# Kernel optimization log

Measured on AMD Instinct MI355X. Metric: run time of the kernel, lower is better.

## Reference

```python
import jax, jax.numpy as jnp
import numpy as np

N = 8192
F_IN = 512
F_OUT = 512
DENSITY = 0.01


def setup_inputs() -> dict:
    key = jax.random.key(0)
    k_x, k_adj, k_w, k_b = jax.random.split(key, 4)
    input_features = jax.random.normal(k_x, (N, F_IN), dtype=jnp.float32)
    adj = (jax.random.uniform(k_adj, (N, N)) < DENSITY).astype(jnp.float32)
    idx = jnp.arange(N)
    adj = adj.at[idx, idx].set(1.0)
    # nn.Linear(in, out) params; W stored as [in, out] so hidden = x @ W + b
    W = jax.random.normal(k_w, (F_IN, F_OUT), dtype=jnp.float32) / np.sqrt(F_IN)
    b = jax.random.normal(k_b, (F_OUT,), dtype=jnp.float32) * 0.01
    return {"input_features": input_features, "adj": adj, "W": W, "b": b}


def reference(input_features, adj, W, b):
    # adj.to_dense().bool().float(): binarize any nonzero entry
    A = (adj != 0).astype(input_features.dtype)  # [N, N]
    hidden = input_features @ W + b              # [N, F_out]
    deg = jnp.sum(A, axis=0)                     # column sums, [N]
    return (A @ hidden) / deg[:, None]           # [N, F_out]
```

## Files before the change

### kernel.cpp

```cpp
#include <hip/hip_runtime.h>
#include <stdint.h>

#define N_NODES 8192
#define FEAT 512
#define QCAP 512

__device__ __forceinline__ unsigned short f2bf(float f) {
  unsigned int u = __float_as_uint(f);
  u += 0x7fffu + ((u >> 16) & 1u);
  return (unsigned short)(u >> 16);
}
__device__ __forceinline__ float bflo(unsigned int u) { return __uint_as_float(u << 16); }
__device__ __forceinline__ float bfhi(unsigned int u) { return __uint_as_float(u & 0xffff0000u); }

typedef __attribute__((ext_vector_type(8))) short short8;
typedef __attribute__((ext_vector_type(4))) float floatx4;

__global__ __launch_bounds__(256) void prep_kernel(const float* __restrict__ W,
                                                   unsigned short* __restrict__ Wt,
                                                   unsigned int* __restrict__ deg) {
  int gid = blockIdx.x * 256 + threadIdx.x;
  int k = gid >> 9, n = gid & 511;
  Wt[n * 512 + k] = f2bf(W[gid]);
  if (gid < N_NODES) deg[gid] = 0u;
}

__global__ __launch_bounds__(512) void gemm_kernel(const float* __restrict__ x,
                                                   const unsigned short* __restrict__ Wt,
                                                   const float* __restrict__ bias,
                                                   unsigned short* __restrict__ hidden) {
  __shared__ __align__(16) unsigned short Ab[64][40];
  __shared__ __align__(16) unsigned short Bb[256][40];
  int t = threadIdx.x;
  int m0 = blockIdx.x * 64;
  int n0 = blockIdx.y * 256;
  int lane = t & 63, wave = t >> 6;
  int quad = lane >> 4, l15 = lane & 15;
  int wm = wave & 1, wn = wave >> 1;

  floatx4 acc[2][4];
#pragma unroll
  for (int i = 0; i < 2; ++i)
#pragma unroll
    for (int j = 0; j < 4; ++j) acc[i][j] = (floatx4)0.0f;

  int ar = t >> 3, ac = (t & 7) * 4;
  int br = t >> 1, bc = (t & 1) * 16;
  const float* xa = x + (size_t)(m0 + ar) * 512 + ac;
  const unsigned short* wb = Wt + (size_t)(n0 + br) * 512 + bc;

  float4 av = *(const float4*)xa;
  uint4 bv0 = *(const uint4*)wb;
  uint4 bv1 = *(const uint4*)(wb + 8);

  for (int kt = 0; kt < 16; ++kt) {
    uint2 aw;
    aw.x = (unsigned int)f2bf(av.x) | ((unsigned int)f2bf(av.y) << 16);
    aw.y = (unsigned int)f2bf(av.z) | ((unsigned int)f2bf(av.w) << 16);
    __syncthreads();
    *(uint2*)&Ab[ar][ac] = aw;
    *(uint4*)&Bb[br][bc] = bv0;
    *(uint4*)&Bb[br][bc + 8] = bv1;
    if (kt < 15) {
      int k0 = (kt + 1) * 32;
      av  = *(const float4*)(xa + k0);
      bv0 = *(const uint4*)(wb + k0);
      bv1 = *(const uint4*)(wb + k0 + 8);
    }
    __syncthreads();

    short8 af[2];
    short8 bfr[4];
#pragma unroll
    for (int im = 0; im < 2; ++im)
      af[im] = *(const short8*)&Ab[wm * 32 + im * 16 + l15][quad * 8];
#pragma unroll
    for (int jn = 0; jn < 4; ++jn)
      bfr[jn] = *(const short8*)&Bb[wn * 64 + jn * 16 + l15][quad * 8];
#pragma unroll
    for (int im = 0; im < 2; ++im)
#pragma unroll
      for (int jn = 0; jn < 4; ++jn)
        acc[im][jn] = __builtin_amdgcn_mfma_f32_16x16x32_bf16(af[im], bfr[jn], acc[im][jn], 0, 0, 0);
  }

#pragma unroll
  for (int jn = 0; jn < 4; ++jn) {
    int col = n0 + wn * 64 + jn * 16 + l15;
    float bb = bias[col];
#pragma unroll
    for (int im = 0; im < 2; ++im) {
#pragma unroll
      for (int rg = 0; rg < 4; ++rg) {
        int row = m0 + wm * 32 + im * 16 + quad * 4 + rg;
        hidden[(size_t)row * 512 + col] = f2bf(acc[im][jn][rg] + bb);
      }
    }
  }
}

__global__ __launch_bounds__(512) void gather_kernel(const float* __restrict__ adj,
                                                     const unsigned short* __restrict__ hidden,
                                                     float* __restrict__ out,
                                                     unsigned int* __restrict__ deg) {
  __shared__ unsigned int degl[N_NODES];
  __shared__ unsigned short q[8][QCAP];
  int tid = threadIdx.x;
#pragma unroll
  for (int i = 0; i < 16; ++i) degl[i * 512 + tid] = 0u;
  __syncthreads();

  int lane = tid & 63, wave = tid >> 6;
  unsigned short* wq = q[wave];
  unsigned long long lanemask = (1ull << lane) - 1ull;
  int r = blockIdx.x * 8 + wave;

  const float4* __restrict__ arow = (const float4*)(adj + ((size_t)r << 13));
  int qcnt = 0;

  float4 c0 = arow[lane];
  float4 c1 = arow[64 + lane];
  for (int ch = 0; ch < 32; ++ch) {
    float4 nx = make_float4(0.f, 0.f, 0.f, 0.f);
    if (ch < 30) nx = arow[(ch + 2) * 64 + lane];
    int cbase = ch * 256 + 4 * lane;
#pragma unroll
    for (int e = 0; e < 4; ++e) {
      float val = (e == 0) ? c0.x : (e == 1) ? c0.y : (e == 2) ? c0.z : c0.w;
      bool nz = (val != 0.0f);
      unsigned long long m = __ballot(nz);
      if (nz) {
        atomicAdd(&degl[cbase + e], 1u);
        wq[qcnt + __popcll(m & lanemask)] = (unsigned short)(cbase + e);
      }
      qcnt += __popcll(m);
    }
    c0 = c1; c1 = nx;
  }

  float acc[8] = {0.f, 0.f, 0.f, 0.f, 0.f, 0.f, 0.f, 0.f};
  int qhead = 0;
  for (; qhead + 8 <= qcnt; qhead += 8) {
    int jj[8];
#pragma unroll
    for (int d = 0; d < 8; ++d) jj[d] = wq[qhead + d];
    uint4 h[8];
#pragma unroll
    for (int d = 0; d < 8; ++d)
      h[d] = ((const uint4*)(hidden + ((size_t)jj[d] << 9)))[lane];
#pragma unroll
    for (int d = 0; d < 8; ++d) {
      acc[0] += bflo(h[d].x); acc[1] += bfhi(h[d].x);
      acc[2] += bflo(h[d].y); acc[3] += bfhi(h[d].y);
      acc[4] += bflo(h[d].z); acc[5] += bfhi(h[d].z);
      acc[6] += bflo(h[d].w); acc[7] += bfhi(h[d].w);
    }
  }
  for (; qhead < qcnt; ++qhead) {
    int j = wq[qhead];
    uint4 h = ((const uint4*)(hidden + ((size_t)j << 9)))[lane];
    acc[0] += bflo(h.x); acc[1] += bfhi(h.x);
    acc[2] += bflo(h.y); acc[3] += bfhi(h.y);
    acc[4] += bflo(h.z); acc[5] += bfhi(h.z);
    acc[6] += bflo(h.w); acc[7] += bfhi(h.w);
  }

  float4* orow = (float4*)(out + ((size_t)r << 9));
  orow[2 * lane]     = make_float4(acc[0], acc[1], acc[2], acc[3]);
  orow[2 * lane + 1] = make_float4(acc[4], acc[5], acc[6], acc[7]);

  __syncthreads();
#pragma unroll
  for (int i = 0; i < 16; ++i) {
    unsigned int c = degl[i * 512 + tid];
    if (c) atomicAdd(&deg[i * 512 + tid], c);
  }
}

__global__ __launch_bounds__(256) void norm_kernel(float* __restrict__ out,
                                                   const unsigned int* __restrict__ deg) {
  int lane = threadIdx.x & 63, wave = threadIdx.x >> 6;
  int r = blockIdx.x * 4 + wave;
  float s = 1.0f / (float)deg[r];
  float4* p = (float4*)(out + ((size_t)r << 9));
  float4 v0 = p[lane], v1 = p[64 + lane];
  v0.x *= s; v0.y *= s; v0.z *= s; v0.w *= s;
  v1.x *= s; v1.y *= s; v1.z *= s; v1.w *= s;
  p[lane] = v0;
  p[64 + lane] = v1;
}

extern "C" void kernel_launch(void* const* d_in, const int* in_sizes, int n_in,
                              void* d_out, int out_size, void* d_ws, size_t ws_size,
                              hipStream_t stream) {
  const float* x   = (const float*)d_in[0];
  const float* adj = (const float*)d_in[1];
  const float* W   = (const float*)d_in[2];
  const float* b   = (const float*)d_in[3];
  float* out = (float*)d_out;

  char* ws = (char*)d_ws;
  unsigned short* hidden = (unsigned short*)ws;
  unsigned short* Wt     = (unsigned short*)(ws + (size_t)N_NODES * FEAT * 2);
  unsigned int*   deg    = (unsigned int*)(ws + (size_t)N_NODES * FEAT * 2 + (size_t)FEAT * FEAT * 2);

  prep_kernel<<<1024, 256, 0, stream>>>(W, Wt, deg);
  gemm_kernel<<<dim3(128, 2), 512, 0, stream>>>(x, Wt, b, hidden);
  gather_kernel<<<1024, 512, 0, stream>>>(adj, hidden, out, deg);
  norm_kernel<<<2048, 256, 0, stream>>>(out, deg);
}
```

Measured before the change: 426.5 us.

## Overlap GEMM with adjacency scan in one launch; fold normalization into gather

Merges the dense GEMM and the adjacency scan into one kernel launch. The first 256 blocks compute hidden while the remaining blocks scan the 256MB adjacency, write per-row neighbor queues to global memory and accumulate degrees. A separate drain kernel then gathers hidden rows and applies the 1/deg scaling directly, which removes the norm kernel and its extra read and write of the output. The aim is to hide the GEMM behind the bandwidth-bound adjacency read. The cost is a round trip of the queues through global memory.

```diff
diff --git a/kernel.cpp b/kernel.cpp
--- a/kernel.cpp
+++ b/kernel.cpp
@@ -25,120 +25,146 @@
   if (gid < N_NODES) deg[gid] = 0u;
 }
 
-__global__ __launch_bounds__(512) void gemm_kernel(const float* __restrict__ x,
-                                                   const unsigned short* __restrict__ Wt,
-                                                   const float* __restrict__ bias,
-                                                   unsigned short* __restrict__ hidden) {
-  __shared__ __align__(16) unsigned short Ab[64][40];
-  __shared__ __align__(16) unsigned short Bb[256][40];
+__global__ __launch_bounds__(512) void fused_kernel(const float* __restrict__ x,
+                                                    const unsigned short* __restrict__ Wt,
+                                                    const float* __restrict__ bias,
+                                                    unsigned short* __restrict__ hidden,
+                                                    const float* __restrict__ adj,
+                                                    unsigned short* __restrict__ gq,
+                                                    unsigned int* __restrict__ qlen,
+                                                    unsigned int* __restrict__ deg) {
+  __shared__ __align__(16) char smem[32768];
+  int b = blockIdx.x;
   int t = threadIdx.x;
-  int m0 = blockIdx.x * 64;
-  int n0 = blockIdx.y * 256;
   int lane = t & 63, wave = t >> 6;
-  int quad = lane >> 4, l15 = lane & 15;
-  int wm = wave & 1, wn = wave >> 1;
-
-  floatx4 acc[2][4];
-#pragma unroll
-  for (int i = 0; i < 2; ++i)
-#pragma unroll
-    for (int j = 0; j < 4; ++j) acc[i][j] = (floatx4)0.0f;
-
-  int ar = t >> 3, ac = (t & 7) * 4;
-  int br = t >> 1, bc = (t & 1) * 16;
-  const float* xa = x + (size_t)(m0 + ar) * 512 + ac;
-  const unsigned short* wb = Wt + (size_t)(n0 + br) * 512 + bc;
-
-  float4 av = *(const float4*)xa;
-  uint4 bv0 = *(const uint4*)wb;
-  uint4 bv1 = *(const uint4*)(wb + 8);
-
-  for (int kt = 0; kt < 16; ++kt) {
-    uint2 aw;
-    aw.x = (unsigned int)f2bf(av.x) | ((unsigned int)f2bf(av.y) << 16);
-    aw.y = (unsigned int)f2bf(av.z) | ((unsigned int)f2bf(av.w) << 16);
+
+  if (b < 256) {
+    unsigned short (*Ab)[40] = (unsigned short (*)[40])smem;
+    unsigned short (*Bb)[40] = (unsigned short (*)[40])(smem + 64 * 40 * 2);
+    int m0 = (b >> 1) * 64;
+    int n0 = (b & 1) * 256;
+    int quad = lane >> 4, l15 = lane & 15;
+    int wm = wave & 1, wn = wave >> 1;
+
+    floatx4 acc[2][4];
+#pragma unroll
+    for (int i = 0; i < 2; ++i)
+#pragma unroll
+      for (int j = 0; j < 4; ++j) acc[i][j] = (floatx4)0.0f;
+
+    int ar = t >> 3, ac = (t & 7) * 4;
+    int br = t >> 1, bc = (t & 1) * 16;
+    const float* xa = x + (size_t)(m0 + ar) * 512 + ac;
+    const unsigned short* wb = Wt + (size_t)(n0 + br) * 512 + bc;
+
+    float4 av = *(const float4*)xa;
+    uint4 bv0 = *(const uint4*)wb;
+    uint4 bv1 = *(const uint4*)(wb + 8);
+
+    for (int kt = 0; kt < 16; ++kt) {
+      uint2 aw;
+      aw.x = (unsigned int)f2bf(av.x) | ((unsigned int)f2bf(av.y) << 16);
+      aw.y = (unsigned int)f2bf(av.z) | ((unsigned int)f2bf(av.w) << 16);
+      __syncthreads();
+      *(uint2*)&Ab[ar][ac] = aw;
+      *(uint4*)&Bb[br][bc] = bv0;
+      *(uint4*)&Bb[br][bc + 8] = bv1;
+      if (kt < 15) {
+        int k0 = (kt + 1) * 32;
+        av  = *(const float4*)(xa + k0);
+        bv0 = *(const uint4*)(wb + k0);
+        bv1 = *(const uint4*)(wb + k0 + 8);
+      }
+      __syncthreads();
+
+      short8 af[2];
+      short8 bfr[4];
+#pragma unroll
+      for (int im = 0; im < 2; ++im)
+        af[im] = *(const short8*)&Ab[wm * 32 + im * 16 + l15][quad * 8];
+#pragma unroll
+      for (int jn = 0; jn < 4; ++jn)
+        bfr[jn] = *(const short8*)&Bb[wn * 64 + jn * 16 + l15][quad * 8];
+#pragma unroll
+      for (int im = 0; im < 2; ++im)
+#pragma unroll
+        for (int jn = 0; jn < 4; ++jn)
+          acc[im][jn] = __builtin_amdgcn_mfma_f32_16x16x32_bf16(af[im], bfr[jn], acc[im][jn], 0, 0, 0);
+    }
+
+#pragma unroll
+    for (int jn = 0; jn < 4; ++jn) {
+      int col = n0 + wn * 64 + jn * 16 + l15;
+      float bb = bias[col];
+#pragma unroll
+      for (int im = 0; im < 2; ++im) {
+#pragma unroll
+        for (int rg = 0; rg < 4; ++rg) {
+          int row = m0 + wm * 32 + im * 16 + quad * 4 + rg;
+          hidden[(size_t)row * 512 + col] = f2bf(acc[im][jn][rg] + bb);
+        }
+      }
+    }
+  } else {
+    unsigned int* degl = (unsigned int*)smem;
+#pragma unroll
+    for (int i = 0; i < 16; ++i) degl[i * 512 + t] = 0u;
     __syncthreads();
-    *(uint2*)&Ab[ar][ac] = aw;
-    *(uint4*)&Bb[br][bc] = bv0;
-    *(uint4*)&Bb[br][bc + 8] = bv1;
-    if (kt < 15) {
-      int k0 = (kt + 1) * 32;
-      av  = *(const float4*)(xa + k0);
-      bv0 = *(const uint4*)(wb + k0);
-      bv1 = *(const uint4*)(wb + k0 + 8);
-    }
+
+    int r = (b - 256) * 8 + wave;
+    unsigned short* wq = gq + (size_t)r * QCAP;
+    unsigned long long lanemask = (1ull << lane) - 1ull;
+    const float4* __restrict__ arow = (const float4*)(adj + ((size_t)r << 13));
+    int qcnt = 0;
+
+    float4 c0 = arow[lane];
+    float4 c1 = arow[64 + lane];
+    for (int ch = 0; ch < 32; ++ch) {
+      float4 nx = make_float4(0.f, 0.f, 0.f, 0.f);
+      if (ch < 30) nx = arow[(ch + 2) * 64 + lane];
+      int cbase = ch * 256 + 4 * lane;
+#pragma unroll
+      for (int e = 0; e < 4; ++e) {
+        float val = (e == 0) ? c0.x : (e == 1) ? c0.y : (e == 2) ? c0.z : c0.w;
+        bool nz = (val != 0.0f);
+        unsigned long long m = __ballot(nz);
+        if (nz) {
+          atomicAdd(&degl[cbase + e], 1u);
+          wq[qcnt + __popcll(m & lanemask)] = (unsigned short)(cbase + e);
+        }
+        qcnt += __popcll(m);
+      }
+      c0 = c1; c1 = nx;
+    }
+    if (lane == 0) qlen[r] = (unsigned int)qcnt;
+
     __syncthreads();
-
-    short8 af[2];
-    short8 bfr[4];
-#pragma unroll
-    for (int im = 0; im < 2; ++im)
-      af[im] = *(const short8*)&Ab[wm * 32 + im * 16 + l15][quad * 8];
-#pragma unroll
-    for (int jn = 0; jn < 4; ++jn)
-      bfr[jn] = *(const short8*)&Bb[wn * 64 + jn * 16 + l15][quad * 8];
-#pragma unroll
-    for (int im = 0; im < 2; ++im)
-#pragma unroll
-      for (int jn = 0; jn < 4; ++jn)
-        acc[im][jn] = __builtin_amdgcn_mfma_f32_16x16x32_bf16(af[im], bfr[jn], acc[im][jn], 0, 0, 0);
+#pragma unroll
+    for (int i = 0; i < 16; ++i) {
+      unsigned int c = degl[i * 512 + t];
+      if (c) atomicAdd(&deg[i * 512 + t], c);
+    }
   }
-
-#pragma unroll
-  for (int jn = 0; jn < 4; ++jn) {
-    int col = n0 + wn * 64 + jn * 16 + l15;
-    float bb = bias[col];
-#pragma unroll
-    for (int im = 0; im < 2; ++im) {
-#pragma unroll
-      for (int rg = 0; rg < 4; ++rg) {
-        int row = m0 + wm * 32 + im * 16 + quad * 4 + rg;
-        hidden[(size_t)row * 512 + col] = f2bf(acc[im][jn][rg] + bb);
-      }
-    }
-  }
-}
-
-__global__ __launch_bounds__(512) void gather_kernel(const float* __restrict__ adj,
-                                                     const unsigned short* __restrict__ hidden,
-                                                     float* __restrict__ out,
-                                                     unsigned int* __restrict__ deg) {
-  __shared__ unsigned int degl[N_NODES];
+}
+
+__global__ __launch_bounds__(512) void drain_kernel(const unsigned short* __restrict__ gq,
+                                                    const unsigned int* __restrict__ qlen,
+                                                    const unsigned short* __restrict__ hidden,
+                                                    const unsigned int* __restrict__ deg,
+                                                    float* __restrict__ out) {
   __shared__ unsigned short q[8][QCAP];
-  int tid = threadIdx.x;
-#pragma unroll
-  for (int i = 0; i < 16; ++i) degl[i * 512 + tid] = 0u;
+  int t = threadIdx.x, lane = t & 63, wave = t >> 6;
+  int r = blockIdx.x * 8 + wave;
+  int qcnt = (int)qlen[r];
+
+  const uint4* src = (const uint4*)(gq + (size_t)r * QCAP);
+  uint4* dst = (uint4*)q[wave];
+  int nv = (qcnt + 7) >> 3;
+  if (lane < nv) dst[lane] = src[lane];
   __syncthreads();
 
-  int lane = tid & 63, wave = tid >> 6;
+  float acc[8] = {0.f, 0.f, 0.f, 0.f, 0.f, 0.f, 0.f, 0.f};
   unsigned short* wq = q[wave];
-  unsigned long long lanemask = (1ull << lane) - 1ull;
-  int r = blockIdx.x * 8 + wave;
-
-  const float4* __restrict__ arow = (const float4*)(adj + ((size_t)r << 13));
-  int qcnt = 0;
-
-  float4 c0 = arow[lane];
-  float4 c1 = arow[64 + lane];
-  for (int ch = 0; ch < 32; ++ch) {
-    float4 nx = make_float4(0.f, 0.f, 0.f, 0.f);
-    if (ch < 30) nx = arow[(ch + 2) * 64 + lane];
-    int cbase = ch * 256 + 4 * lane;
-#pragma unroll
-    for (int e = 0; e < 4; ++e) {
-      float val = (e == 0) ? c0.x : (e == 1) ? c0.y : (e == 2) ? c0.z : c0.w;
-      bool nz = (val != 0.0f);
-      unsigned long long m = __ballot(nz);
-      if (nz) {
-        atomicAdd(&degl[cbase + e], 1u);
-        wq[qcnt + __popcll(m & lanemask)] = (unsigned short)(cbase + e);
-      }
-      qcnt += __popcll(m);
-    }
-    c0 = c1; c1 = nx;
-  }
-
-  float acc[8] = {0.f, 0.f, 0.f, 0.f, 0.f, 0.f, 0.f, 0.f};
   int qhead = 0;
   for (; qhead + 8 <= qcnt; qhead += 8) {
     int jj[8];
@@ -165,29 +191,10 @@
     acc[6] += bflo(h.w); acc[7] += bfhi(h.w);
   }
 
+  float s = 1.0f / (float)deg[r];
   float4* orow = (float4*)(out + ((size_t)r << 9));
-  orow[2 * lane]     = make_float4(acc[0], acc[1], acc[2], acc[3]);
-  orow[2 * lane + 1] = make_float4(acc[4], acc[5], acc[6], acc[7]);
-
-  __syncthreads();
-#pragma unroll
-  for (int i = 0; i < 16; ++i) {
-    unsigned int c = degl[i * 512 + tid];
-    if (c) atomicAdd(&deg[i * 512 + tid], c);
-  }
-}
-
-__global__ __launch_bounds__(256) void norm_kernel(float* __restrict__ out,
-                                                   const unsigned int* __restrict__ deg) {
-  int lane = threadIdx.x & 63, wave = threadIdx.x >> 6;
-  int r = blockIdx.x * 4 + wave;
-  float s = 1.0f / (float)deg[r];
-  float4* p = (float4*)(out + ((size_t)r << 9));
-  float4 v0 = p[lane], v1 = p[64 + lane];
-  v0.x *= s; v0.y *= s; v0.z *= s; v0.w *= s;
-  v1.x *= s; v1.y *= s; v1.z *= s; v1.w *= s;
-  p[lane] = v0;
-  p[64 + lane] = v1;
+  orow[2 * lane]     = make_float4(acc[0] * s, acc[1] * s, acc[2] * s, acc[3] * s);
+  orow[2 * lane + 1] = make_float4(acc[4] * s, acc[5] * s, acc[6] * s, acc[7] * s);
 }
 
 extern "C" void kernel_launch(void* const* d_in, const int* in_sizes, int n_in,
@@ -201,11 +208,12 @@
 
   char* ws = (char*)d_ws;
   unsigned short* hidden = (unsigned short*)ws;
-  unsigned short* Wt     = (unsigned short*)(ws + (size_t)N_NODES * FEAT * 2);
-  unsigned int*   deg    = (unsigned int*)(ws + (size_t)N_NODES * FEAT * 2 + (size_t)FEAT * FEAT * 2);
+  unsigned short* Wt     = (unsigned short*)(ws + (8u << 20));
+  unsigned int*   deg    = (unsigned int*)(ws + (8u << 20) + (512u << 10));
+  unsigned int*   qlen   = (unsigned int*)(ws + (8u << 20) + (544u << 10));
+  unsigned short* gq     = (unsigned short*)(ws + (8u << 20) + (576u << 10));
 
   prep_kernel<<<1024, 256, 0, stream>>>(W, Wt, deg);
-  gemm_kernel<<<dim3(128, 2), 512, 0, stream>>>(x, Wt, b, hidden);
-  gather_kernel<<<1024, 512, 0, stream>>>(adj, hidden, out, deg);
-  norm_kernel<<<2048, 256, 0, stream>>>(out, deg);
-}
+  fused_kernel<<<1280, 512, 0, stream>>>(x, Wt, b, hidden, adj, gq, qlen, deg);
+  drain_kernel<<<1024, 512, 0, stream>>>(gq, qlen, hidden, deg, out);
+}
```

After: 427.1 us. Within noise of the previous version (+0.2%).
